# Optimization experiments

Measured on AMD Instinct MI355X. Metric: run time of the kernel, lower is better.

## Reference

```python
import jax, jax.numpy as jnp
import numpy as np

B, S, D = 4, 2048, 1024
H = 16
HD = D // H

def setup_inputs() -> dict:
    key = jax.random.key(0)
    ks = jax.random.split(key, 6)
    std = 1.0 / np.sqrt(D)
    x = jax.random.normal(ks[0], (B, S, D), dtype=jnp.float32)
    Wq = jax.random.uniform(ks[1], (D, D), jnp.float32, -std, std)
    Wk = jax.random.uniform(ks[2], (D, D), jnp.float32, -std, std)
    Wv = jax.random.uniform(ks[3], (D, D), jnp.float32, -std, std)
    Wo = jax.random.uniform(ks[4], (D, D), jnp.float32, -std, std)
    bo = jax.random.uniform(ks[5], (D,), jnp.float32, -std, std)
    return {"x": x, "Wq": Wq, "Wk": Wk, "Wv": Wv, "Wo": Wo, "bo": bo}

def reference(x, Wq, Wk, Wv, Wo, bo):
    b, s, _ = x.shape
    # projections; torch Linear computes x @ W^T, here W stored as (d_in, d_out)... we use (D, D) applied as x @ W
    q = (x @ Wq).reshape(b, s, H, HD).transpose(0, 2, 1, 3)  # b h s hd
    k = (x @ Wk).reshape(b, s, H, HD).transpose(0, 2, 1, 3)
    v = (x @ Wv).reshape(b, s, H, HD).transpose(0, 2, 1, 3)
    scores = jnp.einsum('bhqd,bhkd->bhqk', q, k)
    causal = jnp.triu(jnp.ones((s, s), dtype=bool), k=1)
    scores = jnp.where(causal[None, None], -jnp.inf, scores)
    attn = jax.nn.softmax(scores / np.sqrt(HD), axis=-1)  # dropout=0.0 -> identity
    ctx = jnp.einsum('bhqk,bhkd->bhqd', attn, v)
    ctx = ctx.transpose(0, 2, 1, 3).reshape(b, s, D)
    return ctx @ Wo + bo
```

## Files before the change

### kernel.cpp

```cpp
#include <hip/hip_runtime.h>

typedef unsigned short u16;
typedef __bf16 bf16x8 __attribute__((ext_vector_type(8)));
typedef float f32x4 __attribute__((ext_vector_type(4)));

#define Bn 4
#define Sn 2048
#define Dn 1024
#define Hn 16
#define HDn 64

__device__ inline u16 f2bf(float f) {
  unsigned u = __builtin_bit_cast(unsigned, f);
  u += 0x7fffu + ((u >> 16) & 1u);
  return (u16)(u >> 16);
}

__device__ __forceinline__ void gl2lds16(const u16* g, u16* l) {
  __builtin_amdgcn_global_load_lds(
      (const __attribute__((address_space(1))) unsigned int*)g,
      (__attribute__((address_space(3))) unsigned int*)l, 16, 0, 0);
}

__device__ __forceinline__ float fexp2(float x) {
  return __builtin_amdgcn_exp2f(x);
}

__device__ __forceinline__ unsigned pk_bf_trunc(float lo, float hi) {
  return __builtin_amdgcn_perm(__builtin_bit_cast(unsigned, hi),
                               __builtin_bit_cast(unsigned, lo), 0x07060302u);
}

__global__ __launch_bounds__(256) void cvt4(const float* __restrict__ in,
                                            u16* __restrict__ out, int n4) {
  int i = blockIdx.x * 256 + threadIdx.x;
  if (i < n4) {
    float4 v = ((const float4*)in)[i];
    ushort4 o;
    o.x = f2bf(v.x); o.y = f2bf(v.y); o.z = f2bf(v.z); o.w = f2bf(v.w);
    ((ushort4*)out)[i] = o;
  }
}

__global__ __launch_bounds__(256) void tcvt4(const float* __restrict__ w0,
                                             const float* __restrict__ w1,
                                             const float* __restrict__ w2,
                                             const float* __restrict__ w3,
                                             u16* __restrict__ out) {
  __shared__ u16 tile[32][33];
  const float* in = (blockIdx.z == 0) ? w0 : (blockIdx.z == 1) ? w1
                   : (blockIdx.z == 2) ? w2 : w3;
  u16* dst = out + (size_t)blockIdx.z * Dn * Dn;
  int bx = blockIdx.x * 32;
  int by = blockIdx.y * 32;
  int tx = threadIdx.x & 31;
  int ty = threadIdx.x >> 5;
#pragma unroll
  for (int r = 0; r < 32; r += 8)
    tile[ty + r][tx] = f2bf(in[(size_t)(by + ty + r) * Dn + bx + tx]);
  __syncthreads();
#pragma unroll
  for (int r = 0; r < 32; r += 8)
    dst[(size_t)(bx + ty + r) * Dn + by + tx] = tile[tx][ty + r];
}

#define MFMA16(a, b, c) __builtin_amdgcn_mfma_f32_16x16x32_bf16(a, b, c, 0, 0, 0)

#define SRCP_INIT(APTR, BPTR)                                                \
  const u16* srcp[3][2];                                                     \
  _Pragma("unroll") for (int rg = 0; rg < 3; rg++) {                         \
    _Pragma("unroll") for (int j = 0; j < 2; j++) {                          \
      int o = j * 8192 + tid * 16;                                           \
      int l = o ^ (((o >> 8) & 7) << 4);                                     \
      int rho = l >> 7;                                                      \
      int c2 = (l >> 1) & 63;                                                \
      int gr;                                                                \
      if (rg == 0)      gr = bm + rho;                                       \
      else if (rg == 1) gr = bn + ((rho >> 5) << 6) + (rho & 31);            \
      else              gr = bn + ((rho >> 5) << 6) + 32 + (rho & 31);       \
      const u16* base = (rg == 0) ? (APTR) : (BPTR);                         \
      srcp[rg][j] = base + (size_t)gr * Dn + c2;                             \
    }                                                                        \
  }

#define ARD(D, Q, F, K)                                                      \
  (*(const bf16x8*)((const char*)&S[D][0][0] +                               \
      ((wr * 64 + (Q) * 32 + (F) * 16 + lcol) * 128 + ((K) ? cs1 : cs0))))
#define BRD(D, NI, K)                                                        \
  (*(const bf16x8*)((const char*)&S[D][1 + ((NI) >> 1)][0] +                 \
      ((wc * 32 + ((NI) & 1) * 16 + lcol) * 128 + ((K) ? cs1 : cs0))))

#define VM6 asm volatile("s_waitcnt vmcnt(6)" ::: "memory")
#define VM0 asm volatile("s_waitcnt vmcnt(0)" ::: "memory")

#define KTILE(D, DN, T, WAIT)                                                \
  {                                                                          \
    stg(0, DN, (T) + 2); stg(1, DN, (T) + 2); stg(2, DN, (T) + 2);           \
    __builtin_amdgcn_sched_barrier(0);                                       \
    bf16x8 a00 = ARD(D, 0, 0, 0), a10 = ARD(D, 0, 1, 0);                     \
    bf16x8 a20 = ARD(D, 1, 0, 0), a30 = ARD(D, 1, 1, 0);                     \
    bf16x8 bk0[4], bk1[4];                                                   \
    _Pragma("unroll") for (int ni = 0; ni < 4; ni++) bk0[ni] = BRD(D, ni, 0);\
    bf16x8 a01 = ARD(D, 0, 0, 1), a11 = ARD(D, 0, 1, 1);                     \
    bf16x8 a21 = ARD(D, 1, 0, 1), a31 = ARD(D, 1, 1, 1);                     \
    _Pragma("unroll") for (int ni = 0; ni < 4; ni++) bk1[ni] = BRD(D, ni, 1);\
    __builtin_amdgcn_s_setprio(1);                                           \
    _Pragma("unroll") for (int ni = 0; ni < 4; ni++) {                       \
      acc[0][ni] = MFMA16(a00, bk0[ni], acc[0][ni]);                         \
      acc[1][ni] = MFMA16(a10, bk0[ni], acc[1][ni]);                         \
      acc[2][ni] = MFMA16(a20, bk0[ni], acc[2][ni]);                         \
      acc[3][ni] = MFMA16(a30, bk0[ni], acc[3][ni]);                         \
    }                                                                        \
    _Pragma("unroll") for (int ni = 0; ni < 4; ni++) {                       \
      acc[0][ni] = MFMA16(a01, bk1[ni], acc[0][ni]);                         \
      acc[1][ni] = MFMA16(a11, bk1[ni], acc[1][ni]);                         \
      acc[2][ni] = MFMA16(a21, bk1[ni], acc[2][ni]);                         \
      acc[3][ni] = MFMA16(a31, bk1[ni], acc[3][ni]);                         \
    }                                                                        \
    __builtin_amdgcn_s_setprio(0);                                           \
    WAIT;                                                                    \
    __builtin_amdgcn_s_barrier();                                            \
    __builtin_amdgcn_sched_barrier(0);                                       \
  }

#define KLOOP                                                                \
  stg(0, 0, 0); stg(1, 0, 0); stg(2, 0, 0);                                  \
  stg(0, 1, 1); stg(1, 1, 1); stg(2, 1, 1);                                  \
  VM6;                                                                       \
  __builtin_amdgcn_s_barrier();                                              \
  __builtin_amdgcn_sched_barrier(0);                                         \
  _Pragma("unroll 1") for (int I = 0; I < 5; ++I) {                          \
    const int T0 = 3 * I;                                                    \
    KTILE(0, 2, T0, VM6)                                                     \
    KTILE(1, 0, T0 + 1, VM6)                                                 \
    KTILE(2, 1, T0 + 2, if (I == 4) { VM0; } else { VM6; })                  \
  }                                                                          \
  KTILE(0, 2, 15, )

__global__ __launch_bounds__(512, 2) void gemm_qkv(const u16* __restrict__ A,
                                                   const u16* __restrict__ Bt,
                                                   u16* __restrict__ qkb,
                                                   u16* __restrict__ vt,
                                                   float qscale) {
  __shared__ __attribute__((aligned(16))) u16 S[3][3][8192];

  const int tid = threadIdx.x;
  const int lane = tid & 63;
  const int lcol = lane & 15;
  const int quad = lane >> 4;
  const int wave = tid >> 6;
  const int wr = wave >> 2;
  const int wc = wave & 3;

  const int bid = blockIdx.x;
  const int idx = bid >> 3;
  const int bm = (((bid & 7) << 3) + (idx & 7)) * 128;
  const int bn = (idx >> 3) * 256;

  SRCP_INIT(A, Bt)

  auto stg = [&](int rg, int buf, int tile) {
    if (tile >= 16) return;
    const int k0 = tile << 6;
    u16* d = &S[buf][rg][tid * 8];
    gl2lds16(srcp[rg][0] + k0, d);
    gl2lds16(srcp[rg][1] + k0, d + 4096);
  };

  f32x4 acc[4][4];
#pragma unroll
  for (int i = 0; i < 4; i++)
#pragma unroll
    for (int j = 0; j < 4; j++) acc[i][j] = (f32x4){0.f, 0.f, 0.f, 0.f};

  const int SW = (lcol & 14) << 3;
  const int cs0 = (quad * 16) ^ SW;
  const int cs1 = (64 + quad * 16) ^ SW;

  KLOOP

  const int rb = bm + wr * 64 + quad * 4;
  const int cb = bn + wc * 64 + lcol;
  if (bn >= 2048) {
#pragma unroll
    for (int mi = 0; mi < 4; mi++) {
#pragma unroll
      for (int ni = 0; ni < 4; ni++) {
        int row0 = rb + mi * 16;
        int s = row0 & (Sn - 1);
        int bb = row0 >> 11;
        int vcol = cb + ni * 16 - 2048;
        int bh = (bb << 4) + (vcol >> 6);
        int hd = vcol & 63;
        unsigned d0 = (unsigned)f2bf(acc[mi][ni][0]) |
                      ((unsigned)f2bf(acc[mi][ni][1]) << 16);
        unsigned d1 = (unsigned)f2bf(acc[mi][ni][2]) |
                      ((unsigned)f2bf(acc[mi][ni][3]) << 16);
        *(uint2*)(vt + ((size_t)bh * HDn + hd) * Sn + s) = (uint2){d0, d1};
      }
    }
  } else {
    const float scale = (bn < 1024) ? qscale : 1.0f;
#pragma unroll
    for (int mi = 0; mi < 4; mi++) {
#pragma unroll
      for (int ni = 0; ni < 4; ni++) {
        int row0 = rb + mi * 16;
        int col = cb + ni * 16;
#pragma unroll
        for (int r = 0; r < 4; r++)
          qkb[(size_t)(row0 + r) * 2048 + col] = f2bf(acc[mi][ni][r] * scale);
      }
    }
  }
}

__global__ __launch_bounds__(512, 2) void gemm_out(const u16* __restrict__ A,
                                                   const u16* __restrict__ Bt,
                                                   float* __restrict__ Cout,
                                                   const float* __restrict__ bias) {
  __shared__ __attribute__((aligned(16))) u16 S[3][3][8192];

  const int tid = threadIdx.x;
  const int lane = tid & 63;
  const int lcol = lane & 15;
  const int quad = lane >> 4;
  const int wave = tid >> 6;
  const int wr = wave >> 2;
  const int wc = wave & 3;

  const int bid = blockIdx.x;
  const int idx = bid >> 3;
  const int bm = (((bid & 7) << 3) + (idx & 7)) * 128;
  const int bn = (idx >> 3) * 256;

  SRCP_INIT(A, Bt)

  auto stg = [&](int rg, int buf, int tile) {
    if (tile >= 16) return;
    const int k0 = tile << 6;
    u16* d = &S[buf][rg][tid * 8];
    gl2lds16(srcp[rg][0] + k0, d);
    gl2lds16(srcp[rg][1] + k0, d + 4096);
  };

  f32x4 acc[4][4];
#pragma unroll
  for (int i = 0; i < 4; i++)
#pragma unroll
    for (int j = 0; j < 4; j++) acc[i][j] = (f32x4){0.f, 0.f, 0.f, 0.f};

  const int SW = (lcol & 14) << 3;
  const int cs0 = (quad * 16) ^ SW;
  const int cs1 = (64 + quad * 16) ^ SW;

  KLOOP

  const int rb = bm + wr * 64 + quad * 4;
  const int cb = bn + wc * 64 + lcol;
  float bv[4];
#pragma unroll
  for (int ni = 0; ni < 4; ni++) bv[ni] = bias[cb + ni * 16];
#pragma unroll
  for (int mi = 0; mi < 4; mi++) {
#pragma unroll
    for (int ni = 0; ni < 4; ni++) {
      int row0 = rb + mi * 16;
      int col = cb + ni * 16;
#pragma unroll
      for (int r = 0; r < 4; r++)
        Cout[(size_t)(row0 + r) * Dn + col] = acc[mi][ni][r] + bv[ni];
    }
  }
}

__global__ __launch_bounds__(256, 2) void attn5(const u16* __restrict__ QK,
                                                const u16* __restrict__ Vt,
                                                u16* __restrict__ ctx) {
  __shared__ __attribute__((aligned(16))) u16 Ks2[2][2][64][32];
  __shared__ __attribute__((aligned(16))) u16 Vts2[2][2][64][32];
  __shared__ __attribute__((aligned(16))) u16 Pt[4][32][72];

  const int bh = blockIdx.x;
  const int b = bh >> 4, h = bh & 15;
  const int pair = blockIdx.y;
  const int t = threadIdx.x;
  const int w = t >> 6;
  const int lane = t & 63;
  const int lcol = lane & 15;
  const int quad = lane >> 4;
  const int qw0 = pair * 128 + w * 32;
  const int qw1 = (15 - pair) * 128 + w * 32;

  const size_t qkbase = ((size_t)b * Sn) * 2048 + h * HDn;
  const size_t obase = ((size_t)b * Sn) * Dn + h * HDn;
  const size_t vbase = ((size_t)bh * HDn) * Sn;

  bf16x8 qf[2][2][2];
#pragma unroll
  for (int si = 0; si < 2; si++) {
    const int qws = si ? qw1 : qw0;
#pragma unroll
    for (int qb = 0; qb < 2; qb++) {
      const u16* qp = QK + qkbase + (size_t)(qws + qb * 16 + lcol) * 2048 + quad * 8;
      qf[si][qb][0] = *(const bf16x8*)qp;
      qf[si][qb][1] = *(const bf16x8*)(qp + 32);
    }
  }

  f32x4 o[2][2][4];
#pragma unroll
  for (int si = 0; si < 2; si++)
#pragma unroll
    for (int qb = 0; qb < 2; qb++)
#pragma unroll
      for (int nb = 0; nb < 4; nb++) o[si][qb][nb] = (f32x4){0.f, 0.f, 0.f, 0.f};
  float lsum[2][2] = {{0.f, 0.f}, {0.f, 0.f}};

  const int srow = lane >> 2;
  const int sseg = ((lane & 3) ^ ((lane >> 3) & 3)) * 8;
  const u16* kp0 = QK + qkbase + 1024 + (size_t)(w * 16 + srow) * 2048 + sseg;
  const u16* vp0 = Vt + vbase + (size_t)(w * 16 + srow) * Sn + sseg;
  u16* ksl = &Ks2[0][0][0][0] + w * 512 + lane * 8;
  u16* vsl = &Vts2[0][0][0][0] + w * 512 + lane * 8;

  const int rsw = (quad ^ ((lcol >> 1) & 3)) * 8;

  auto stg_kv = [&](int bs, int j0) {
    const u16* kp = kp0 + (size_t)j0 * 2048;
    const u16* vp = vp0 + j0;
    u16* kd = ksl + bs * 4096;
    u16* vd = vsl + bs * 4096;
    gl2lds16(kp, kd);
    gl2lds16(kp + 32, kd + 2048);
    gl2lds16(vp, vd);
    gl2lds16(vp + 32, vd + 2048);
  };

  auto do_strip = [&](int si, int qw, int j0, int bs) {
    f32x4 s[4][2];
#pragma unroll
    for (int mb = 0; mb < 4; mb++) {
      bf16x8 kf0 = *(const bf16x8*)(&Ks2[bs][0][mb * 16 + lcol][rsw]);
      bf16x8 kf1 = *(const bf16x8*)(&Ks2[bs][1][mb * 16 + lcol][rsw]);
#pragma unroll
      for (int qb = 0; qb < 2; qb++) {
        f32x4 a = (f32x4){0.f, 0.f, 0.f, 0.f};
        a = __builtin_amdgcn_mfma_f32_16x16x32_bf16(kf0, qf[si][qb][0], a, 0, 0, 0);
        a = __builtin_amdgcn_mfma_f32_16x16x32_bf16(kf1, qf[si][qb][1], a, 0, 0, 0);
        s[mb][qb] = a;
      }
    }

    const bool needmask = (j0 + 63 > qw);
#pragma unroll
    for (int qb = 0; qb < 2; qb++) {
      const int qrow = qw + qb * 16 + lcol;
#pragma unroll
      for (int mb = 0; mb < 4; mb++) {
        float p[4];
#pragma unroll
        for (int r = 0; r < 4; r++) p[r] = fexp2(s[mb][qb][r]);
        if (needmask) {
          const int kvb = j0 + mb * 16 + quad * 4;
#pragma unroll
          for (int r = 0; r < 4; r++)
            if (kvb + r > qrow) p[r] = 0.f;
        }
        lsum[si][qb] += (p[0] + p[1]) + (p[2] + p[3]);
        unsigned d0 = pk_bf_trunc(p[0], p[1]);
        unsigned d1 = pk_bf_trunc(p[2], p[3]);
        *(uint2*)(&Pt[w][qb * 16 + lcol][mb * 16 + quad * 4]) = (uint2){d0, d1};
      }
    }

#pragma unroll
    for (int c = 0; c < 2; c++) {
      bf16x8 pf0 = *(const bf16x8*)(&Pt[w][lcol][c * 32 + quad * 8]);
      bf16x8 pf1 = *(const bf16x8*)(&Pt[w][16 + lcol][c * 32 + quad * 8]);
#pragma unroll
      for (int nb = 0; nb < 4; nb++) {
        bf16x8 vf = *(const bf16x8*)(&Vts2[bs][c][nb * 16 + lcol][rsw]);
        o[si][0][nb] = __builtin_amdgcn_mfma_f32_16x16x32_bf16(vf, pf0, o[si][0][nb], 0, 0, 0);
        o[si][1][nb] = __builtin_amdgcn_mfma_f32_16x16x32_bf16(vf, pf1, o[si][1][nb], 0, 0, 0);
      }
    }
  };

  const int n_kv = (15 - pair) * 128 + 128;
  const int nit = n_kv >> 6;

  stg_kv(0, 0);
#pragma unroll 1
  for (int it = 0; it < nit; ++it) {
    const int j0 = it << 6;
    const int bs = it & 1;
    if (it + 1 < nit) {
      stg_kv(bs ^ 1, j0 + 64);
      asm volatile("s_waitcnt vmcnt(4)" ::: "memory");
    } else {
      asm volatile("s_waitcnt vmcnt(0)" ::: "memory");
    }
    __builtin_amdgcn_s_barrier();
    __builtin_amdgcn_sched_barrier(0);

    if (j0 <= qw1 + 31) do_strip(1, qw1, j0, bs);
    if (j0 <= qw0 + 31) do_strip(0, qw0, j0, bs);

    __builtin_amdgcn_s_barrier();
    __builtin_amdgcn_sched_barrier(0);
  }

#pragma unroll
  for (int si = 0; si < 2; si++) {
    const int qws = si ? qw1 : qw0;
#pragma unroll
    for (int qb = 0; qb < 2; qb++) {
      float l = lsum[si][qb];
      l += __shfl_xor(l, 16);
      l += __shfl_xor(l, 32);
      float inv = 1.0f / l;
#pragma unroll
      for (int nb = 0; nb < 4; nb++) {
        unsigned d0 = (unsigned)f2bf(o[si][qb][nb][0] * inv) |
                      ((unsigned)f2bf(o[si][qb][nb][1] * inv) << 16);
        unsigned d1 = (unsigned)f2bf(o[si][qb][nb][2] * inv) |
                      ((unsigned)f2bf(o[si][qb][nb][3] * inv) << 16);
        u16* p = ctx + obase + (size_t)(qws + qb * 16 + lcol) * Dn + nb * 16 + quad * 4;
        *(uint2*)p = (uint2){d0, d1};
      }
    }
  }
}

extern "C" void kernel_launch(void* const* d_in, const int* in_sizes, int n_in,
                              void* d_out, int out_size, void* d_ws, size_t ws_size,
                              hipStream_t stream) {
  const float* x  = (const float*)d_in[0];
  const float* Wq = (const float*)d_in[1];
  const float* Wk = (const float*)d_in[2];
  const float* Wv = (const float*)d_in[3];
  const float* Wo = (const float*)d_in[4];
  const float* bo = (const float*)d_in[5];
  float* out = (float*)d_out;

  const size_t BSD = (size_t)Bn * Sn * Dn;
  const size_t DD = (size_t)Dn * Dn;

  u16* xb    = (u16*)d_ws;
  u16* wall  = xb + BSD;
  u16* qkb   = wall + 4 * DD;
  u16* vt    = qkb + 2 * BSD;
  u16* cb    = vt + BSD;

  cvt4<<<(int)(BSD / 4 / 256), 256, 0, stream>>>(x, xb, (int)(BSD / 4));
  tcvt4<<<dim3(Dn / 32, Dn / 32, 4), 256, 0, stream>>>(Wq, Wk, Wv, Wo, wall);

  gemm_qkv<<<dim3(768), 512, 0, stream>>>(xb, wall, qkb, vt,
                                          0.125f * 1.44269504f);

  attn5<<<dim3(Bn * Hn, 8), 256, 0, stream>>>(qkb, vt, cb);

  gemm_out<<<dim3(256), 512, 0, stream>>>(cb, wall + 3 * DD, out, bo);
}
```

Measured before the change: 237.9 us.

## Interleave QK, softmax and PV phases across strips and compute row sums via MFMA

Splits the per-strip attention body into separate QK, softmax and PV phases and interleaves the two query strips so MFMA work from one strip can overlap the exp/packing VALU work of the other. The P buffer in LDS is doubled so both strips can hold probabilities at once. Row sums are now computed by an extra MFMA against a ones vector instead of VALU adds plus cross-lane shuffles, and s_setprio raises wave priority around the MFMA phases. This costs more LDS and registers (two score tiles live at once), which may reduce occupancy. Row sums are now taken from the bf16-truncated probabilities, the same values used for PV.

```diff
diff --git a/kernel.cpp b/kernel.cpp
--- a/kernel.cpp
+++ b/kernel.cpp
@@ -279,7 +279,7 @@
                                                 u16* __restrict__ ctx) {
   __shared__ __attribute__((aligned(16))) u16 Ks2[2][2][64][32];
   __shared__ __attribute__((aligned(16))) u16 Vts2[2][2][64][32];
-  __shared__ __attribute__((aligned(16))) u16 Pt[4][32][72];
+  __shared__ __attribute__((aligned(16))) u16 Pt[2][4][32][72];
 
   const int bh = blockIdx.x;
   const int b = bh >> 4, h = bh & 15;
@@ -308,14 +308,21 @@
     }
   }
 
+  bf16x8 onesf;
+#pragma unroll
+  for (int i = 0; i < 8; i++) onesf[i] = (__bf16)1.0f;
+
   f32x4 o[2][2][4];
-#pragma unroll
-  for (int si = 0; si < 2; si++)
-#pragma unroll
-    for (int qb = 0; qb < 2; qb++)
+  f32x4 ls[2][2];
+#pragma unroll
+  for (int si = 0; si < 2; si++) {
+#pragma unroll
+    for (int qb = 0; qb < 2; qb++) {
+      ls[si][qb] = (f32x4){0.f, 0.f, 0.f, 0.f};
 #pragma unroll
       for (int nb = 0; nb < 4; nb++) o[si][qb][nb] = (f32x4){0.f, 0.f, 0.f, 0.f};
-  float lsum[2][2] = {{0.f, 0.f}, {0.f, 0.f}};
+    }
+  }
 
   const int srow = lane >> 2;
   const int sseg = ((lane & 3) ^ ((lane >> 3) & 3)) * 8;
@@ -337,8 +344,8 @@
     gl2lds16(vp + 32, vd + 2048);
   };
 
-  auto do_strip = [&](int si, int qw, int j0, int bs) {
-    f32x4 s[4][2];
+  auto qk_strip = [&](int si, f32x4 (*s)[2], int bs) {
+    __builtin_amdgcn_s_setprio(1);
 #pragma unroll
     for (int mb = 0; mb < 4; mb++) {
       bf16x8 kf0 = *(const bf16x8*)(&Ks2[bs][0][mb * 16 + lcol][rsw]);
@@ -346,12 +353,15 @@
 #pragma unroll
       for (int qb = 0; qb < 2; qb++) {
         f32x4 a = (f32x4){0.f, 0.f, 0.f, 0.f};
-        a = __builtin_amdgcn_mfma_f32_16x16x32_bf16(kf0, qf[si][qb][0], a, 0, 0, 0);
-        a = __builtin_amdgcn_mfma_f32_16x16x32_bf16(kf1, qf[si][qb][1], a, 0, 0, 0);
+        a = MFMA16(kf0, qf[si][qb][0], a);
+        a = MFMA16(kf1, qf[si][qb][1], a);
         s[mb][qb] = a;
       }
     }
-
+    __builtin_amdgcn_s_setprio(0);
+  };
+
+  auto sm_strip = [&](int si, int qw, int j0, f32x4 (*s)[2]) {
     const bool needmask = (j0 + 63 > qw);
 #pragma unroll
     for (int qb = 0; qb < 2; qb++) {
@@ -367,24 +377,29 @@
           for (int r = 0; r < 4; r++)
             if (kvb + r > qrow) p[r] = 0.f;
         }
-        lsum[si][qb] += (p[0] + p[1]) + (p[2] + p[3]);
         unsigned d0 = pk_bf_trunc(p[0], p[1]);
         unsigned d1 = pk_bf_trunc(p[2], p[3]);
-        *(uint2*)(&Pt[w][qb * 16 + lcol][mb * 16 + quad * 4]) = (uint2){d0, d1};
-      }
-    }
-
+        *(uint2*)(&Pt[si][w][qb * 16 + lcol][mb * 16 + quad * 4]) = (uint2){d0, d1};
+      }
+    }
+  };
+
+  auto pv_strip = [&](int si, int bs) {
+    __builtin_amdgcn_s_setprio(1);
 #pragma unroll
     for (int c = 0; c < 2; c++) {
-      bf16x8 pf0 = *(const bf16x8*)(&Pt[w][lcol][c * 32 + quad * 8]);
-      bf16x8 pf1 = *(const bf16x8*)(&Pt[w][16 + lcol][c * 32 + quad * 8]);
+      bf16x8 pf0 = *(const bf16x8*)(&Pt[si][w][lcol][c * 32 + quad * 8]);
+      bf16x8 pf1 = *(const bf16x8*)(&Pt[si][w][16 + lcol][c * 32 + quad * 8]);
+      ls[si][0] = MFMA16(onesf, pf0, ls[si][0]);
+      ls[si][1] = MFMA16(onesf, pf1, ls[si][1]);
 #pragma unroll
       for (int nb = 0; nb < 4; nb++) {
         bf16x8 vf = *(const bf16x8*)(&Vts2[bs][c][nb * 16 + lcol][rsw]);
-        o[si][0][nb] = __builtin_amdgcn_mfma_f32_16x16x32_bf16(vf, pf0, o[si][0][nb], 0, 0, 0);
-        o[si][1][nb] = __builtin_amdgcn_mfma_f32_16x16x32_bf16(vf, pf1, o[si][1][nb], 0, 0, 0);
-      }
-    }
+        o[si][0][nb] = MFMA16(vf, pf0, o[si][0][nb]);
+        o[si][1][nb] = MFMA16(vf, pf1, o[si][1][nb]);
+      }
+    }
+    __builtin_amdgcn_s_setprio(0);
   };
 
   const int n_kv = (15 - pair) * 128 + 128;
@@ -404,8 +419,14 @@
     __builtin_amdgcn_s_barrier();
     __builtin_amdgcn_sched_barrier(0);
 
-    if (j0 <= qw1 + 31) do_strip(1, qw1, j0, bs);
-    if (j0 <= qw0 + 31) do_strip(0, qw0, j0, bs);
+    const bool a0 = (j0 <= qw0 + 31);
+    f32x4 s1[4][2], s0[4][2];
+    qk_strip(1, s1, bs);
+    if (a0) qk_strip(0, s0, bs);
+    sm_strip(1, qw1, j0, s1);
+    if (a0) sm_strip(0, qw0, j0, s0);
+    pv_strip(1, bs);
+    if (a0) pv_strip(0, bs);
 
     __builtin_amdgcn_s_barrier();
     __builtin_amdgcn_sched_barrier(0);
@@ -416,10 +437,7 @@
     const int qws = si ? qw1 : qw0;
 #pragma unroll
     for (int qb = 0; qb < 2; qb++) {
-      float l = lsum[si][qb];
-      l += __shfl_xor(l, 16);
-      l += __shfl_xor(l, 32);
-      float inv = 1.0f / l;
+      float inv = 1.0f / ls[si][qb][0];
 #pragma unroll
       for (int nb = 0; nb < 4; nb++) {
         unsigned d0 = (unsigned)f2bf(o[si][qb][nb][0] * inv) |
```

Result: no change. 233.9 us (-1.7%).
